# Performance work log

Measured on AMD Instinct MI355X. Metric: run time of the kernel, lower is better.

The kernel has to match this reference:

```python
import jax, jax.numpy as jnp
import numpy as np

LN_EPS = 1e-5
NEG_SLOPE = 0.01  # torch LeakyReLU default
H, D = 16, 64


def _layernorm(x, g, b):
    m = jnp.mean(x, axis=-1, keepdims=True)
    v = jnp.var(x, axis=-1, keepdims=True)
    return (x - m) * jax.lax.rsqrt(v + LN_EPS) * g + b


def _mlp(x, ln_g, ln_b, W1, b1, W2, b2):
    h = _layernorm(x, ln_g, ln_b)
    h = jax.nn.gelu(h @ W1 + b1, approximate=False)
    return h @ W2 + b2


def _gather_nodes(node_msg, edge_index):
    # node_msg: (b,n,c), edge_index: (b,n,k) -> (b,n,k,c)
    return jax.vmap(lambda nm, ei: nm[ei])(node_msg, edge_index)


def setup_inputs() -> dict:
    key = jax.random.key(0)
    ks = jax.random.split(key, 16)
    b, n, k = 2, 1024, 32
    dim, pdim, msg_dim = 512, 256, 256
    s = 0.02
    inp = {
        'node_repr': jax.random.normal(ks[0], (b, n, dim), jnp.float32),
        'edge_repr': jax.random.normal(ks[1], (b, n, k, pdim), jnp.float32),
        'edge_index': jax.random.randint(ks[2], (b, n, k), 0, n, jnp.int32),
        'edge_mask': jax.random.randint(ks[3], (b, n, k), 0, 2, jnp.int32),
        'mask_bw': jnp.ones((b, n, k, 1), jnp.float32),
        'W_edge_msg': s * jax.random.normal(ks[4], (pdim, msg_dim), jnp.float32),
        'W_node_src': s * jax.random.normal(ks[5], (dim, msg_dim), jnp.float32),
        'W_node_tgt': s * jax.random.normal(ks[6], (dim, msg_dim), jnp.float32),
        'msg_ln_g': jnp.ones((msg_dim,), jnp.float32),
        'msg_ln_b': jnp.zeros((msg_dim,), jnp.float32),
        'msg_W1': s * jax.random.normal(ks[7], (msg_dim, 4 * msg_dim), jnp.float32),
        'msg_b1': jnp.zeros((4 * msg_dim,), jnp.float32),
        'msg_W2': s * jax.random.normal(ks[8], (4 * msg_dim, msg_dim), jnp.float32),
        'msg_b2': jnp.zeros((msg_dim,), jnp.float32),
        'W_gate': jnp.zeros((dim, msg_dim), jnp.float32),   # init_weights: zeros
        'b_gate': -jnp.ones((msg_dim,), jnp.float32),       # init_weights: -1
        'W_out': s * jax.random.normal(ks[9], (msg_dim, dim), jnp.float32),
        'W_msg': s * jax.random.normal(ks[10], (msg_dim, msg_dim), jnp.float32),
        'W_attn_bias': s * jax.random.normal(ks[11], (msg_dim, H), jnp.float32),
        'W_gat_value': s * jax.random.normal(ks[12], (msg_dim, H * D), jnp.float32),
        'W_gat_gate': jnp.zeros((dim, H * D), jnp.float32),
        'b_gat_gate': -jnp.ones((H * D,), jnp.float32),
        'W_gat_out': s * jax.random.normal(ks[13], (H * D, dim), jnp.float32),
        'node_ln_g': jnp.ones((dim,), jnp.float32),
        'node_ln_b': jnp.zeros((dim,), jnp.float32),
        'node_W1': s * jax.random.normal(ks[14], (dim, 4 * dim), jnp.float32),
        'node_b1': jnp.zeros((4 * dim,), jnp.float32),
        'node_W2': s * jax.random.normal(ks[15], (4 * dim, dim), jnp.float32),
        'node_b2': jnp.zeros((dim,), jnp.float32),
    }
    return inp


def reference(node_repr, edge_repr, edge_index, edge_mask, mask_bw,
              W_edge_msg, W_node_src, W_node_tgt,
              msg_ln_g, msg_ln_b, msg_W1, msg_b1, msg_W2, msg_b2,
              W_gate, b_gate, W_out,
              W_msg, W_attn_bias, W_gat_value, W_gat_gate, b_gat_gate, W_gat_out,
              node_ln_g, node_ln_b, node_W1, node_b1, node_W2, node_b2):
    b, n, k = edge_index.shape
    em_bool = edge_mask.astype(bool)          # (b,n,k)
    em_f = edge_mask.astype(node_repr.dtype)

    # edge-wise message: edge proj + gathered src node proj + broadcast tgt node proj
    node_msg = node_repr @ W_node_src                      # (b,n,msg)
    msg = edge_repr @ W_edge_msg \
        + _gather_nodes(node_msg, edge_index) * mask_bw \
        + (node_repr @ W_node_tgt)[:, :, None, :]          # (b,n,k,msg)
    msg = _mlp(msg, msg_ln_g, msg_ln_b, msg_W1, msg_b1, msg_W2, msg_b2)
    msg = jnp.where(em_bool[..., None], msg, 0.0)

    # global (mean-pooled, gated) path
    o = (msg * em_f[..., None]).sum(-2) / (em_f.sum(-1, keepdims=True) + 1e-6)
    o = jax.nn.sigmoid(node_repr @ W_gate + b_gate) * o
    dh = o @ W_out                                         # (b,n,dim)

    # GAT path: per-node attention over its k neighbors
    ab = jnp.where(NEG_SLOPE < 1, jax.nn.leaky_relu(msg @ W_msg, NEG_SLOPE), msg) @ W_attn_bias  # (b,n,k,H)
    ab = jnp.where(em_bool[..., None], ab, -jnp.finfo(ab.dtype).max)
    attn = jax.nn.softmax(ab, axis=2)                      # softmax over k
    v = (msg @ W_gat_value).reshape(b, n, k, H, D)
    og = jnp.einsum('bnkh,bnkhd->bnhd', attn, v).reshape(b, n, H * D)
    og = jax.nn.sigmoid(node_repr @ W_gat_gate + b_gat_gate) * og
    dh = dh + og @ W_gat_out

    # residual + node MLP (dropout is identity in eval mode)
    node_repr = node_repr + dh
    node_repr = node_repr + _mlp(node_repr, node_ln_g, node_ln_b, node_W1, node_b1, node_W2, node_b2)
    return node_repr
```

## Files before the change

### kernel.cpp

```cpp
#include <hip/hip_runtime.h>
#include <hip/hip_bf16.h>

typedef unsigned short u16;
typedef short s16x8 __attribute__((ext_vector_type(8)));
typedef float f32x4 __attribute__((ext_vector_type(4)));
typedef float f32x8 __attribute__((ext_vector_type(8)));
typedef u16 u16x8 __attribute__((ext_vector_type(8)));

#define DEV static __device__ __forceinline__

DEV float b2f(u16 u){ unsigned int i=((unsigned int)u)<<16; float f; __builtin_memcpy(&f,&i,4); return f; }
DEV u16 f2b(float x){ __hip_bfloat16 h=__float2bfloat16(x); u16 u; __builtin_memcpy(&u,&h,2); return u; }
DEV f32x4 MFMA(s16x8 a, s16x8 b, f32x4 c){ return __builtin_amdgcn_mfma_f32_16x16x32_bf16(a,b,c,0,0,0); }
DEV s16x8 LD8(const u16* p){ return *(const s16x8*)p; }
DEV float gelu_fast(float x){
  float u = 0.7978845608f*(x + 0.044715f*x*x*x);
  float e = __expf(2.f*u);
  float th = 1.f - 2.f/(e + 1.f);
  return 0.5f*x*(1.f + th);
}
DEV float sigmf(float x){ return 1.0f/(1.0f+__expf(-x)); }

DEV void gload16(const u16* g, u16* l){
  __builtin_amdgcn_global_load_lds((const __attribute__((address_space(1))) void*)g,
                                   (__attribute__((address_space(3))) void*)l, 16, 0, 0);
}

#define WS_WeT   0
#define WS_W1T   65536
#define WS_W2T   327680
#define WS_WmT   589824
#define WS_WvT   655360
#define WS_WoT   917504
#define WS_WgoT  1048576
#define WS_nW1T  1572864
#define WS_nW2T  2621440
#define WS_SrcT  3670016
#define WS_TgtT  3801088
#define WS_GateT 3932160
#define WS_GgT   4063232
#define WS_NM    4587520
#define WS_TGT   5111808
#define WS_GP    5636096
#define WS_GG    6160384
#define WS_MSG   8257536
#define WS_U2    8257536
#define WS_X     10354688
#define WS_Y     12451840
#define WS_WM    25034752
#define WS_U1    33423360
#define WS_YE    33947648
#define WS_H     50724864

struct P13 { const float* p[13]; };
__device__ const int TR_START[14] = {0,16,80,144,160,224,256,384,640,896,928,960,992,1120};
__device__ const int TR_R[13]   = {256,256,1024,256,256,256,1024,512,2048,512,512,512,512};
__device__ const int TR_C[13]   = {256,1024,256,256,1024,512,512,2048,512,256,256,256,1024};
__device__ const int TR_DST[13] = {WS_WeT,WS_W1T,WS_W2T,WS_WmT,WS_WvT,WS_WoT,WS_WgoT,
                                   WS_nW1T,WS_nW2T,WS_SrcT,WS_TgtT,WS_GateT,WS_GgT};

__global__ __launch_bounds__(256) void k_transpose(P13 ps, u16* __restrict__ ws){
  __shared__ alignas(16) u16 Ts[64][72];
  const int t = threadIdx.x;
  int bid = blockIdx.x;
  int mi = 0;
  #pragma unroll 1
  while (bid >= TR_START[mi+1]) ++mi;
  const float* src = ps.p[mi];
  const int R = TR_R[mi], C = TR_C[mi];
  u16* dst = ws + TR_DST[mi];
  const int ti = bid - TR_START[mi];
  const int tcn = C >> 6;
  const int tr = ti / tcn, tc = ti % tcn;
  {
    const int row = t >> 2, cs = (t & 3) * 16;
    const float* sp = src + (tr*64 + row)*C + tc*64 + cs;
    u16x8 a, b;
    #pragma unroll
    for (int i=0;i<8;i++){ a[i]=f2b(sp[i]); b[i]=f2b(sp[8+i]); }
    *(u16x8*)&Ts[row][cs]   = a;
    *(u16x8*)&Ts[row][cs+8] = b;
  }
  __syncthreads();
  {
    const int col = t >> 2, rs = (t & 3) * 16;
    u16x8 a, b;
    #pragma unroll
    for (int i=0;i<8;i++){ a[i]=Ts[rs+i][col]; b[i]=Ts[rs+8+i][col]; }
    u16* dp = dst + (tc*64 + col)*R + tr*64 + rs;
    *(u16x8*)dp = a;
    *(u16x8*)(dp+8) = b;
  }
}

__global__ __launch_bounds__(256) void k_cvtnode(const float* __restrict__ src, u16* __restrict__ dst){
  const int i = (blockIdx.x*256 + threadIdx.x)*8;
  f32x8 v = *(const f32x8*)(src + i);
  u16x8 o;
  #pragma unroll
  for (int j=0;j<8;j++) o[j] = f2b(v[j]);
  *(u16x8*)(dst + i) = o;
}

__global__ __launch_bounds__(256) void k_proj(const float* __restrict__ bgate,
                                              const float* __restrict__ bgg,
                                              u16* __restrict__ ws){
  const int t=threadIdx.x, lid=t&63, w=t>>6, g=lid>>4, q=lid&15;
  const int rb = blockIdx.x, yb = blockIdx.y;
  const u16* nb = ws + WS_H;
  const u16* BT; u16* dst; int Nseg, colbase, act=0; const float* bias=nullptr;
  if (yb < 4){ BT=ws+WS_SrcT;  dst=ws+WS_NM; Nseg=256;  colbase=yb*64; }
  else if (yb < 8){ BT=ws+WS_TgtT;  dst=ws+WS_TGT; Nseg=256; colbase=(yb-4)*64; }
  else if (yb < 12){ BT=ws+WS_GateT; dst=ws+WS_GP; Nseg=256; colbase=(yb-8)*64; act=1; bias=bgate; }
  else { BT=ws+WS_GgT; dst=ws+WS_GG; Nseg=1024; colbase=(yb-12)*64; act=1; bias=bgg; }
  const int wr=(w>>1)*32, wcl=(w&1)*32;
  f32x4 acc[2][2] = {};
  for (int kk=0; kk<512; kk+=32){
    s16x8 af[2], bfr[2];
    #pragma unroll
    for (int i=0;i<2;i++) af[i] = LD8(nb + (rb*64 + wr + i*16 + q)*512 + kk + 8*g);
    #pragma unroll
    for (int j=0;j<2;j++) bfr[j] = LD8(BT + (colbase + wcl + j*16 + q)*512 + kk + 8*g);
    #pragma unroll
    for (int i=0;i<2;i++)
      #pragma unroll
      for (int j=0;j<2;j++) acc[i][j] = MFMA(af[i], bfr[j], acc[i][j]);
  }
  #pragma unroll
  for (int i=0;i<2;i++)
    #pragma unroll
    for (int j=0;j<2;j++)
      #pragma unroll
      for (int r=0;r<4;r++){
        const int row = rb*64 + wr + i*16 + g*4 + r;
        const int col = wcl + j*16 + q;
        float v = acc[i][j][r];
        if (act) v = sigmf(v + bias[colbase+col]);
        dst[row*Nseg + colbase + col] = f2b(v);
      }
}

#define GB_S 528
__global__ __launch_bounds__(256) void k_edgepre(
    const float* __restrict__ edge_repr, const int* __restrict__ edge_index,
    const float* __restrict__ mask_bw,
    const float* __restrict__ ln_g, const float* __restrict__ ln_b,
    u16* __restrict__ ws)
{
  __shared__ alignas(16) char SH[64*GB_S];
  __shared__ float rsS[4][64], rsQ[4][64];
  __shared__ int idxL[64]; __shared__ float mbwL[64];

  const int t=threadIdx.x, lid=t&63, w=t>>6, g=lid>>4, q=lid&15;
  const int R0 = blockIdx.x * 64;
  const int wc = w * 64;
  u16* As = (u16*)SH;
  u16* Bs = (u16*)(SH + 4096);

  if (t < 64){
    idxL[t] = edge_index[R0+t];
    mbwL[t] = mask_bw[R0+t];
  }
  __syncthreads();

  const u16* nm = ws + WS_NM;
  const u16* tg = ws + WS_TGT;
  #pragma unroll
  for (int it=0; it<8; ++it){
    const int v = t + 256*it;
    const int row = v >> 5;
    const int sc  = (v & 31) * 8;
    const int er  = R0 + row;
    const int gnd = er >> 5;
    const int bi  = gnd >> 10;
    const int srow = bi*1024 + idxL[row];
    const float mb = mbwL[row];
    u16x8 nv = *(const u16x8*)(nm + srow*256 + sc);
    u16x8 tv = *(const u16x8*)(tg + gnd*256 + sc);
    u16x8 ov;
    #pragma unroll
    for (int j2=0;j2<8;j2++) ov[j2] = f2b(b2f(nv[j2])*mb + b2f(tv[j2]));
    *(u16x8*)(SH + row*GB_S + 2*sc) = ov;
  }
  __syncthreads();
  f32x4 acc[4][4];
  #pragma unroll
  for (int i=0;i<4;i++)
    #pragma unroll
    for (int r=0;r<4;r++){
      const int row = i*16 + g*4 + r;
      #pragma unroll
      for (int j=0;j<4;j++){
        const int col = wc + j*16 + q;
        acc[i][j][r] = b2f(*(const u16*)(SH + row*GB_S + 2*col));
      }
    }
  for (int kk=0; kk<256; kk+=32){
    __syncthreads();
    {
      const int row = t >> 2, c0 = (t & 3) * 8;
      const float* sp = edge_repr + (R0 + row)*256 + kk + c0;
      f32x8 fv = *(const f32x8*)sp;
      u16x8 av;
      #pragma unroll
      for (int j2=0;j2<8;j2++) av[j2] = f2b(fv[j2]);
      *(u16x8*)(As + row*32 + c0) = av;
    }
    #pragma unroll
    for (int j=0;j<4;j++){
      const int s = t + 256*j;
      const int brow = s >> 2, ko = (s & 3) * 8;
      u16* ldsB = Bs + (w*64 + 256*j)*8;
      gload16(ws + WS_WeT + brow*256 + kk + ko, ldsB);
    }
    __syncthreads();
    s16x8 af[4], bfr[4];
    #pragma unroll
    for (int i=0;i<4;i++) af[i]  = *(const s16x8*)(As + (i*16+q)*32 + g*8);
    #pragma unroll
    for (int j=0;j<4;j++) bfr[j] = *(const s16x8*)(Bs + (wc + j*16 + q)*32 + g*8);
    #pragma unroll
    for (int i=0;i<4;i++)
      #pragma unroll
      for (int j=0;j<4;j++) acc[i][j] = MFMA(af[i], bfr[j], acc[i][j]);
  }
  #pragma unroll
  for (int i=0;i<4;i++)
    #pragma unroll
    for (int r=0;r<4;r++){
      float s=0.f, s2=0.f;
      #pragma unroll
      for (int j=0;j<4;j++){ float v=acc[i][j][r]; s+=v; s2+=v*v; }
      #pragma unroll
      for (int m=1;m<16;m<<=1){ s += __shfl_xor(s,m,64); s2 += __shfl_xor(s2,m,64); }
      if (q==0){ const int row=i*16+g*4+r; rsS[w][row]=s; rsQ[w][row]=s2; }
    }
  __syncthreads();
  u16* Ye = ws + WS_YE;
  #pragma unroll
  for (int i=0;i<4;i++)
    #pragma unroll
    for (int r=0;r<4;r++){
      const int row=i*16+g*4+r;
      const float s  = rsS[0][row]+rsS[1][row]+rsS[2][row]+rsS[3][row];
      const float s2 = rsQ[0][row]+rsQ[1][row]+rsQ[2][row]+rsQ[3][row];
      const float mean = s*(1.f/256.f);
      const float var  = s2*(1.f/256.f) - mean*mean;
      const float rstd = rsqrtf(var + 1e-5f);
      #pragma unroll
      for (int j=0;j<4;j++){
        const int col = wc + j*16 + q;
        Ye[(R0+row)*256 + col] = f2b((acc[i][j][r]-mean)*rstd*ln_g[col] + ln_b[col]);
      }
    }
}

__global__ __launch_bounds__(256) void k_mlp1(const u16* __restrict__ A,
                                              const u16* __restrict__ BT,
                                              const float* __restrict__ b1,
                                              u16* __restrict__ H){
  __shared__ alignas(16) u16 SH2[64*136];
  u16* As = SH2;
  u16* Bs = SH2 + 4096;
  const int t=threadIdx.x, lid=t&63, w=t>>6, g=lid>>4, q=lid&15;
  const int r0 = blockIdx.x*128, n0 = blockIdx.y*128;
  const int wc3 = w*32;
  f32x4 acc[8][2] = {};
  for (int kk=0;kk<256;kk+=32){
    __syncthreads();
    #pragma unroll
    for (int j=0;j<2;j++){
      const int v = t + 256*j;
      const int row = v>>2, sg = (v&3)*8;
      gload16(A  + (r0+row)*256 + kk + sg, As + (w*64 + 256*j)*8);
      gload16(BT + (n0+row)*256 + kk + sg, Bs + (w*64 + 256*j)*8);
    }
    __syncthreads();
    s16x8 bf_[2];
    #pragma unroll
    for (int j=0;j<2;j++) bf_[j] = *(const s16x8*)(Bs + (wc3 + j*16 + q)*32 + g*8);
    #pragma unroll
    for (int i=0;i<8;i++){
      s16x8 af = *(const s16x8*)(As + (i*16+q)*32 + g*8);
      #pragma unroll
      for (int j=0;j<2;j++) acc[i][j] = MFMA(af, bf_[j], acc[i][j]);
    }
  }
  #pragma unroll
  for (int p=0;p<2;p++){
    __syncthreads();
    #pragma unroll
    for (int i2=0;i2<4;i2++)
      #pragma unroll
      for (int j=0;j<2;j++)
        #pragma unroll
        for (int r=0;r<4;r++){
          const int rl = i2*16 + g*4 + r;
          const int cl = wc3 + j*16 + q;
          SH2[rl*136 + cl] = f2b(gelu_fast(acc[p*4+i2][j][r] + b1[n0 + cl]));
        }
    __syncthreads();
    #pragma unroll
    for (int it=0; it<4; ++it){
      const int v = t + 256*it;
      const int rrow = v >> 4, sc = (v & 15)*8;
      *(u16x8*)(H + (r0 + p*64 + rrow)*1024 + n0 + sc) = *(const u16x8*)(SH2 + rrow*136 + sc);
    }
  }
}

__global__ __launch_bounds__(256) void k_mlp2(const u16* __restrict__ A,
                                              const u16* __restrict__ BT,
                                              const float* __restrict__ b2,
                                              const int* __restrict__ em,
                                              u16* __restrict__ msg){
  __shared__ alignas(16) u16 As[128*32];
  __shared__ alignas(16) u16 Bs[128*32];
  __shared__ int emL[128];
  const int t=threadIdx.x, lid=t&63, w=t>>6, g=lid>>4, q=lid&15;
  const int r0 = blockIdx.x*128, n0 = blockIdx.y*128;
  const int wr=(w>>1)*64, wc2=(w&1)*64;
  if (t < 128) emL[t] = em[r0 + t];
  f32x4 acc[4][4] = {};
  for (int kk=0;kk<1024;kk+=32){
    __syncthreads();
    #pragma unroll
    for (int j=0;j<2;j++){
      const int v = t + 256*j;
      const int row = v>>2, sg = (v&3)*8;
      gload16(A  + (r0+row)*1024 + kk + sg, As + (w*64 + 256*j)*8);
      gload16(BT + (n0+row)*1024 + kk + sg, Bs + (w*64 + 256*j)*8);
    }
    __syncthreads();
    s16x8 af[4], bf_[4];
    #pragma unroll
    for (int i=0;i<4;i++) af[i]  = *(const s16x8*)(As + (wr+i*16+q)*32 + g*8);
    #pragma unroll
    for (int j=0;j<4;j++) bf_[j] = *(const s16x8*)(Bs + (wc2+j*16+q)*32 + g*8);
    #pragma unroll
    for (int i=0;i<4;i++)
      #pragma unroll
      for (int j=0;j<4;j++) acc[i][j] = MFMA(af[i], bf_[j], acc[i][j]);
  }
  #pragma unroll
  for (int i=0;i<4;i++)
    #pragma unroll
    for (int j=0;j<4;j++)
      #pragma unroll
      for (int r=0;r<4;r++){
        const int rl  = wr + i*16 + g*4 + r;
        const int col = n0 + wc2 + j*16 + q;
        float v = acc[i][j][r] + b2[col];
        if (!emL[rl]) v = 0.f;
        msg[(r0+rl)*256 + col] = f2b(v);
      }
}

__global__ __launch_bounds__(256) void k_tm(const u16* __restrict__ A,
                                            const u16* __restrict__ BT,
                                            u16* __restrict__ Tm){
  __shared__ alignas(16) u16 SH2[64*136];
  u16* As = SH2;
  u16* Bs = SH2 + 4096;
  const int t=threadIdx.x, lid=t&63, w=t>>6, g=lid>>4, q=lid&15;
  const int r0 = blockIdx.x*128, n0 = blockIdx.y*128;
  const int wc3 = w*32;
  f32x4 acc[8][2] = {};
  for (int kk=0;kk<256;kk+=32){
    __syncthreads();
    #pragma unroll
    for (int j=0;j<2;j++){
      const int v = t + 256*j;
      const int row = v>>2, sg = (v&3)*8;
      gload16(A  + (r0+row)*256 + kk + sg, As + (w*64 + 256*j)*8);
      gload16(BT + (n0+row)*256 + kk + sg, Bs + (w*64 + 256*j)*8);
    }
    __syncthreads();
    s16x8 bf_[2];
    #pragma unroll
    for (int j=0;j<2;j++) bf_[j] = *(const s16x8*)(Bs + (wc3 + j*16 + q)*32 + g*8);
    #pragma unroll
    for (int i=0;i<8;i++){
      s16x8 af = *(const s16x8*)(As + (i*16+q)*32 + g*8);
      #pragma unroll
      for (int j=0;j<2;j++) acc[i][j] = MFMA(af, bf_[j], acc[i][j]);
    }
  }
  #pragma unroll
  for (int p=0;p<2;p++){
    __syncthreads();
    #pragma unroll
    for (int i2=0;i2<4;i2++)
      #pragma unroll
      for (int j=0;j<2;j++)
        #pragma unroll
        for (int r=0;r<4;r++){
          const int rl = i2*16 + g*4 + r;
          const int cl = wc3 + j*16 + q;
          float v = acc[p*4+i2][j][r];
          SH2[rl*136 + cl] = f2b(v > 0.f ? v : 0.01f*v);
        }
    __syncthreads();
    #pragma unroll
    for (int it=0; it<4; ++it){
      const int v = t + 256*it;
      const int rrow = v >> 4, sc = (v & 15)*8;
      *(u16x8*)(Tm + (r0 + p*64 + rrow)*256 + n0 + sc) = *(const u16x8*)(SH2 + rrow*136 + sc);
    }
  }
}

__global__ __launch_bounds__(256) void k_ab(const u16* __restrict__ A,
                                            const float* __restrict__ Wab,
                                            float* __restrict__ AB){
  __shared__ alignas(16) u16 As[128*32];
  __shared__ alignas(16) char WbT[16*528];
  const int t=threadIdx.x, lid=t&63, w=t>>6, g=lid>>4, q=lid&15;
  const int r0 = blockIdx.x*128;
  {
    const float* wr_ = Wab + t*16;
    #pragma unroll
    for (int h=0;h<16;h++) *(u16*)(WbT + h*528 + 2*t) = f2b(wr_[h]);
  }
  f32x4 acc[2] = {};
  for (int kk=0;kk<256;kk+=32){
    __syncthreads();
    #pragma unroll
    for (int j=0;j<2;j++){
      const int s = t + 256*j;
      const int row = s>>2, ko = (s&3)*8;
      gload16(A + (r0+row)*256 + kk + ko, As + (w*64 + 256*j)*8);
    }
    __syncthreads();
    s16x8 bf_ = *(const s16x8*)(WbT + q*528 + 2*(kk + 8*g));
    #pragma unroll
    for (int i=0;i<2;i++){
      s16x8 af = *(const s16x8*)(As + (w*32 + i*16 + q)*32 + g*8);
      acc[i] = MFMA(af, bf_, acc[i]);
    }
  }
  #pragma unroll
  for (int i=0;i<2;i++)
    #pragma unroll
    for (int r=0;r<4;r++){
      const int row = r0 + w*32 + i*16 + g*4 + r;
      AB[row*16 + q] = acc[i][r];
    }
}

#define AM_S 528
#define MT_S 80
__global__ __launch_bounds__(256) void k_attn2(const int* __restrict__ edge_mask,
                                               u16* __restrict__ ws){
  __shared__ alignas(16) char Am[32*AM_S];
  __shared__ alignas(16) char Mt[256*MT_S];
  __shared__ alignas(16) char Pb[16*80];
  __shared__ float Pp[32][16];
  __shared__ int emL[32];
  __shared__ float cntS;

  const int t=threadIdx.x, lid=t&63, w=t>>6, g=lid>>4, q=lid&15;
  const int nd = blockIdx.x;
  const int wc = w*64;
  const u16* msg = ws + WS_MSG + nd*32*256;
  const float* ab = (const float*)(ws + WS_YE) + nd*32*16;

  if (t < 32) emL[t] = edge_mask[nd*32 + t];
  #pragma unroll
  for (int it=0; it<4; ++it){
    const int v = t + 256*it;
    const int row = v >> 5, sc = (v & 31)*8;
    u16x8 val = *(const u16x8*)(msg + row*256 + sc);
    *(u16x8*)(Am + row*AM_S + 2*sc) = val;
  }
  {
    const int k = t >> 4, h = t & 15;
    Pp[k][h]    = ab[k*16 + h];
    Pp[k+16][h] = ab[(k+16)*16 + h];
  }
  __syncthreads();
  if (t == 0){ float c=0.f; for (int k=0;k<32;k++) c += emL[k]?1.f:0.f; cntS=c; }
  {
    const int c = t;
    #pragma unroll 1
    for (int k=0;k<32;k++){
      u16 vv = *(const u16*)(Am + k*AM_S + 2*c);
      *(u16*)(Mt + c*MT_S + 2*k) = vv;
    }
  }
  if (t < 16){
    const int h = t;
    float m = -3.4028235e38f;
    float pv[32];
    for (int k=0;k<32;k++){ pv[k] = emL[k] ? Pp[k][h] : -3.4028235e38f; m = fmaxf(m, pv[k]); }
    float s = 0.f;
    float ev[32];
    for (int k=0;k<32;k++){ ev[k]=__expf(pv[k]-m); s+=ev[k]; }
    const float inv = 1.f/s;
    for (int k=0;k<32;k++) *(u16*)(Pb + h*80 + 2*k) = f2b(ev[k]*inv);
  }
  __syncthreads();
  {
    s16x8 pa = *(const s16x8*)(Pb + q*80 + 2*(8*g));
    f32x4 wmac[4] = {};
    #pragma unroll
    for (int j=0;j<4;j++){
      s16x8 mb = *(const s16x8*)(Mt + (wc + j*16 + q)*MT_S + 2*(8*g));
      wmac[j] = MFMA(pa, mb, wmac[j]);
    }
    u16* wmw = ws + WS_WM;
    #pragma unroll
    for (int j=0;j<4;j++)
      #pragma unroll
      for (int r=0;r<4;r++){
        const int hh = g*4 + r;
        const int col = wc + j*16 + q;
        wmw[hh*(2048*256) + nd*256 + col] = f2b(wmac[j][r]);
      }
  }
  {
    const int c = t;
    float s = 0.f;
    #pragma unroll 1
    for (int k=0;k<32;k++) s += b2f(*(const u16*)(Am + k*AM_S + 2*c));
    const float o = s / (cntS + 1e-6f);
    ws[WS_U1 + nd*256 + c] = f2b(o * b2f(ws[WS_GP + nd*256 + c]));
  }
}

__global__ __launch_bounds__(256) void k_og(u16* __restrict__ ws){
  const int t=threadIdx.x, lid=t&63, w=t>>6, g=lid>>4, q=lid&15;
  const int rb=blockIdx.x, h=blockIdx.y;
  const int wr=(w>>1)*32, wcl=(w&1)*32;
  const u16* A  = ws + WS_WM  + h*(2048*256);
  const u16* BT = ws + WS_WvT;
  f32x4 acc[2][2] = {};
  for (int kk=0;kk<256;kk+=32){
    s16x8 af[2], bfr[2];
    #pragma unroll
    for (int i=0;i<2;i++) af[i] = LD8(A + (rb*64 + wr + i*16 + q)*256 + kk + 8*g);
    #pragma unroll
    for (int j=0;j<2;j++) bfr[j] = LD8(BT + (h*64 + wcl + j*16 + q)*256 + kk + 8*g);
    #pragma unroll
    for (int i=0;i<2;i++)
      #pragma unroll
      for (int j=0;j<2;j++) acc[i][j] = MFMA(af[i], bfr[j], acc[i][j]);
  }
  #pragma unroll
  for (int i=0;i<2;i++)
    #pragma unroll
    for (int j=0;j<2;j++)
      #pragma unroll
      for (int r=0;r<4;r++){
        const int row = rb*64 + wr + i*16 + g*4 + r;
        const int col = h*64 + wcl + j*16 + q;
        const float gv = b2f(ws[WS_GG + row*1024 + col]);
        ws[WS_U2 + row*1024 + col] = f2b(acc[i][j][r] * gv);
      }
}

__global__ __launch_bounds__(256) void k_dh(const float* __restrict__ node_repr, u16* __restrict__ ws){
  const int t=threadIdx.x, lid=t&63, w=t>>6, g=lid>>4, q=lid&15;
  const int rb=blockIdx.x, cb=blockIdx.y*64;
  const int wr=(w>>1)*32, wcl=(w&1)*32;
  float* Xf = (float*)(ws + WS_X);
  f32x4 acc[2][2] = {};
  for (int kk=0;kk<256;kk+=32){
    s16x8 af[2], bfr[2];
    #pragma unroll
    for (int i=0;i<2;i++) af[i] = LD8(ws + WS_U1 + (rb*64 + wr + i*16 + q)*256 + kk + 8*g);
    #pragma unroll
    for (int j=0;j<2;j++) bfr[j] = LD8(ws + WS_WoT + (cb + wcl + j*16 + q)*256 + kk + 8*g);
    #pragma unroll
    for (int i=0;i<2;i++)
      #pragma unroll
      for (int j=0;j<2;j++) acc[i][j] = MFMA(af[i], bfr[j], acc[i][j]);
  }
  for (int kk=0;kk<1024;kk+=32){
    s16x8 af[2], bfr[2];
    #pragma unroll
    for (int i=0;i<2;i++) af[i] = LD8(ws + WS_U2 + (rb*64 + wr + i*16 + q)*1024 + kk + 8*g);
    #pragma unroll
    for (int j=0;j<2;j++) bfr[j] = LD8(ws + WS_WgoT + (cb + wcl + j*16 + q)*1024 + kk + 8*g);
    #pragma unroll
    for (int i=0;i<2;i++)
      #pragma unroll
      for (int j=0;j<2;j++) acc[i][j] = MFMA(af[i], bfr[j], acc[i][j]);
  }
  #pragma unroll
  for (int i=0;i<2;i++)
    #pragma unroll
    for (int j=0;j<2;j++)
      #pragma unroll
      for (int r=0;r<4;r++){
        const int row = rb*64 + wr + i*16 + g*4 + r;
        const int col = cb + wcl + j*16 + q;
        Xf[row*512 + col] = acc[i][j][r] + node_repr[row*512 + col];
      }
}

__global__ __launch_bounds__(256) void k_ln512(const float* __restrict__ g_, const float* __restrict__ b_,
                                               u16* __restrict__ ws){
  const int t=threadIdx.x, wid=t>>6, lane=t&63;
  const int row = blockIdx.x*4 + wid;
  const float* xr = (const float*)(ws + WS_X) + row*512;
  f32x8 xv = *(const f32x8*)(xr + lane*8);
  float s=0.f, s2=0.f;
  #pragma unroll
  for (int i=0;i<8;i++){ s+=xv[i]; s2+=xv[i]*xv[i]; }
  #pragma unroll
  for (int m=1;m<64;m<<=1){ s += __shfl_xor(s,m,64); s2 += __shfl_xor(s2,m,64); }
  const float mean = s*(1.f/512.f);
  const float var  = s2*(1.f/512.f) - mean*mean;
  const float rstd = rsqrtf(var + 1e-5f);
  u16x8 yv;
  #pragma unroll
  for (int i=0;i<8;i++) yv[i] = f2b((xv[i]-mean)*rstd*g_[lane*8+i] + b_[lane*8+i]);
  *(u16x8*)(ws + WS_Y + row*512 + lane*8) = yv;
}

__global__ __launch_bounds__(256) void k_nmlp1(const u16* __restrict__ A,
                                               const u16* __restrict__ BT,
                                               const float* __restrict__ b1,
                                               u16* __restrict__ H){
  __shared__ alignas(16) u16 SH2[64*136];
  u16* As = SH2;
  u16* Bs = SH2 + 4096;
  const int t=threadIdx.x, lid=t&63, w=t>>6, g=lid>>4, q=lid&15;
  const int r0 = blockIdx.x*128, n0 = blockIdx.y*128;
  const int wc3 = w*32;
  f32x4 acc[8][2] = {};
  for (int kk=0;kk<512;kk+=32){
    __syncthreads();
    #pragma unroll
    for (int j=0;j<2;j++){
      const int v = t + 256*j;
      const int row = v>>2, sg = (v&3)*8;
      gload16(A  + (r0+row)*512 + kk + sg, As + (w*64 + 256*j)*8);
      gload16(BT + (n0+row)*512 + kk + sg, Bs + (w*64 + 256*j)*8);
    }
    __syncthreads();
    s16x8 bf_[2];
    #pragma unroll
    for (int j=0;j<2;j++) bf_[j] = *(const s16x8*)(Bs + (wc3 + j*16 + q)*32 + g*8);
    #pragma unroll
    for (int i=0;i<8;i++){
      s16x8 af = *(const s16x8*)(As + (i*16+q)*32 + g*8);
      #pragma unroll
      for (int j=0;j<2;j++) acc[i][j] = MFMA(af, bf_[j], acc[i][j]);
    }
  }
  #pragma unroll
  for (int p=0;p<2;p++){
    __syncthreads();
    #pragma unroll
    for (int i2=0;i2<4;i2++)
      #pragma unroll
      for (int j=0;j<2;j++)
        #pragma unroll
        for (int r=0;r<4;r++){
          const int rl = i2*16 + g*4 + r;
          const int cl = wc3 + j*16 + q;
          SH2[rl*136 + cl] = f2b(gelu_fast(acc[p*4+i2][j][r] + b1[n0 + cl]));
        }
    __syncthreads();
    #pragma unroll
    for (int it=0; it<4; ++it){
      const int v = t + 256*it;
      const int rrow = v >> 4, sc = (v & 15)*8;
      *(u16x8*)(H + (r0 + p*64 + rrow)*2048 + n0 + sc) = *(const u16x8*)(SH2 + rrow*136 + sc);
    }
  }
}

__global__ __launch_bounds__(256) void k_nmlp2(const u16* __restrict__ A,
                                               const u16* __restrict__ BT,
                                               const float* __restrict__ b2,
                                               const float* __restrict__ Xf,
                                               float* __restrict__ out){
  __shared__ alignas(16) u16 As[64*32];
  __shared__ alignas(16) u16 Bs[64*32];
  const int t=threadIdx.x, lid=t&63, w=t>>6, g=lid>>4, q=lid&15;
  const int r0 = blockIdx.x*64, n0 = blockIdx.y*64;
  const int wr=(w>>1)*32, wc2=(w&1)*32;
  f32x4 acc[2][2] = {};
  for (int kk=0;kk<2048;kk+=32){
    __syncthreads();
    {
      const int row = t>>2, sg = (t&3)*8;
      gload16(A  + (r0+row)*2048 + kk + sg, As + (w*64)*8);
      gload16(BT + (n0+row)*2048 + kk + sg, Bs + (w*64)*8);
    }
    __syncthreads();
    s16x8 af[2], bf_[2];
    #pragma unroll
    for (int i=0;i<2;i++) af[i]  = *(const s16x8*)(As + (wr+i*16+q)*32 + g*8);
    #pragma unroll
    for (int j=0;j<2;j++) bf_[j] = *(const s16x8*)(Bs + (wc2+j*16+q)*32 + g*8);
    #pragma unroll
    for (int i=0;i<2;i++)
      #pragma unroll
      for (int j=0;j<2;j++) acc[i][j] = MFMA(af[i], bf_[j], acc[i][j]);
  }
  #pragma unroll
  for (int i=0;i<2;i++)
    #pragma unroll
    for (int j=0;j<2;j++)
      #pragma unroll
      for (int r=0;r<4;r++){
        const int row = r0 + wr + i*16 + g*4 + r;
        const int col = n0 + wc2 + j*16 + q;
        out[row*512 + col] = acc[i][j][r] + b2[col] + Xf[row*512 + col];
      }
}

extern "C" void kernel_launch(void* const* d_in, const int* in_sizes, int n_in,
                              void* d_out, int out_size, void* d_ws, size_t ws_size,
                              hipStream_t stream){
  (void)in_sizes; (void)n_in; (void)out_size; (void)ws_size;
  const float* node_repr = (const float*)d_in[0];
  const float* edge_repr = (const float*)d_in[1];
  const int* edge_index = (const int*)d_in[2];
  const int* edge_mask  = (const int*)d_in[3];
  const float* mask_bw = (const float*)d_in[4];
  u16* ws = (u16*)d_ws;

  P13 ps;
  const int srcIdx[13] = {5,10,12,17,19,16,22,25,27,6,7,14,20};
  for (int i=0;i<13;i++) ps.p[i] = (const float*)d_in[srcIdx[i]];

  hipLaunchKernelGGL(k_transpose, dim3(1120), dim3(256), 0, stream, ps, ws);
  hipLaunchKernelGGL(k_cvtnode, dim3(512), dim3(256), 0, stream, node_repr, ws + WS_H);
  hipLaunchKernelGGL(k_proj, dim3(32,28), dim3(256), 0, stream,
                     (const float*)d_in[15], (const float*)d_in[21], ws);
  hipLaunchKernelGGL(k_edgepre, dim3(1024), dim3(256), 0, stream,
                     edge_repr, edge_index, mask_bw,
                     (const float*)d_in[8], (const float*)d_in[9], ws);
  for (int grp=0; grp<2; ++grp){
    const u16* Ag = ws + WS_YE + grp*32768*256;
    u16* Hg = ws + WS_H;
    u16* msgg = ws + WS_MSG + grp*32768*256;
    const int* emg = edge_mask + grp*32768;
    hipLaunchKernelGGL(k_mlp1, dim3(256,8), dim3(256), 0, stream,
                       Ag, ws + WS_W1T, (const float*)d_in[11], Hg);
    hipLaunchKernelGGL(k_mlp2, dim3(256,2), dim3(256), 0, stream,
                       Hg, ws + WS_W2T, (const float*)d_in[13], emg, msgg);
  }
  hipLaunchKernelGGL(k_tm, dim3(512,2), dim3(256), 0, stream,
                     ws + WS_MSG, ws + WS_WmT, ws + WS_H);
  hipLaunchKernelGGL(k_ab, dim3(512), dim3(256), 0, stream,
                     ws + WS_H, (const float*)d_in[18], (float*)(ws + WS_YE));
  hipLaunchKernelGGL(k_attn2, dim3(2048), dim3(256), 0, stream,
                     edge_mask, ws);
  hipLaunchKernelGGL(k_og, dim3(32,16), dim3(256), 0, stream, ws);
  hipLaunchKernelGGL(k_dh, dim3(32,8), dim3(256), 0, stream, node_repr, ws);
  hipLaunchKernelGGL(k_ln512, dim3(512), dim3(256), 0, stream,
                     (const float*)d_in[23], (const float*)d_in[24], ws);
  hipLaunchKernelGGL(k_nmlp1, dim3(16,16), dim3(256), 0, stream,
                     ws + WS_Y, ws + WS_nW1T, (const float*)d_in[26], ws + WS_H);
  hipLaunchKernelGGL(k_nmlp2, dim3(32,8), dim3(256), 0, stream,
                     ws + WS_H, ws + WS_nW2T, (const float*)d_in[28],
                     (const float*)(ws + WS_X), (float*)d_out);
}
```

Baseline: 351.8 us.

## Double-buffer edge-projection GEMM loads and stage LayerNorm output through LDS

The k_edgepre K-loop now double-buffers its A (edge_repr converted to bf16) and B (W_edge transposed) tiles in shared memory. The next tile's global loads are issued before the current MFMAs, which leaves one barrier per iteration instead of two. The LayerNorm epilogue writes its bf16 results into LDS first and then copies them out with coalesced 16-byte stores, replacing scattered 2-byte global stores. Shared memory per block grows to about 40 KB, which may reduce occupancy.

```diff
diff --git a/kernel.cpp b/kernel.cpp
--- a/kernel.cpp
+++ b/kernel.cpp
@@ -141,21 +141,22 @@
 }
 
 #define GB_S 528
+#define SH_BYTES 40960
 __global__ __launch_bounds__(256) void k_edgepre(
     const float* __restrict__ edge_repr, const int* __restrict__ edge_index,
     const float* __restrict__ mask_bw,
     const float* __restrict__ ln_g, const float* __restrict__ ln_b,
     u16* __restrict__ ws)
 {
-  __shared__ alignas(16) char SH[64*GB_S];
+  __shared__ alignas(16) char SH[SH_BYTES];
   __shared__ float rsS[4][64], rsQ[4][64];
   __shared__ int idxL[64]; __shared__ float mbwL[64];
 
   const int t=threadIdx.x, lid=t&63, w=t>>6, g=lid>>4, q=lid&15;
   const int R0 = blockIdx.x * 64;
   const int wc = w * 64;
-  u16* As = (u16*)SH;
-  u16* Bs = (u16*)(SH + 4096);
+  u16* AsP = (u16*)SH;
+  u16* BsP = (u16*)SH + 4096;
 
   if (t < 64){
     idxL[t] = edge_index[R0+t];
@@ -195,34 +196,55 @@
         acc[i][j][r] = b2f(*(const u16*)(SH + row*GB_S + 2*col));
       }
     }
-  for (int kk=0; kk<256; kk+=32){
-    __syncthreads();
-    {
-      const int row = t >> 2, c0 = (t & 3) * 8;
-      const float* sp = edge_repr + (R0 + row)*256 + kk + c0;
-      f32x8 fv = *(const f32x8*)sp;
-      u16x8 av;
-      #pragma unroll
-      for (int j2=0;j2<8;j2++) av[j2] = f2b(fv[j2]);
-      *(u16x8*)(As + row*32 + c0) = av;
-    }
+  __syncthreads();
+
+  const int arow = t >> 2, ac0 = (t & 3) * 8;
+  {
+    f32x8 fv = *(const f32x8*)(edge_repr + (R0 + arow)*256 + ac0);
+    u16x8 av;
+    #pragma unroll
+    for (int j2=0;j2<8;j2++) av[j2] = f2b(fv[j2]);
+    *(u16x8*)(AsP + arow*32 + ac0) = av;
     #pragma unroll
     for (int j=0;j<4;j++){
       const int s = t + 256*j;
       const int brow = s >> 2, ko = (s & 3) * 8;
-      u16* ldsB = Bs + (w*64 + 256*j)*8;
-      gload16(ws + WS_WeT + brow*256 + kk + ko, ldsB);
-    }
-    __syncthreads();
+      gload16(ws + WS_WeT + brow*256 + ko, BsP + (w*64 + 256*j)*8);
+    }
+  }
+  __syncthreads();
+  int cur = 0;
+  for (int kk=0; kk<256; kk+=32){
+    const int nxt = cur ^ 1;
+    f32x8 fv;
+    if (kk < 224){
+      fv = *(const f32x8*)(edge_repr + (R0 + arow)*256 + kk + 32 + ac0);
+      #pragma unroll
+      for (int j=0;j<4;j++){
+        const int s = t + 256*j;
+        const int brow = s >> 2, ko = (s & 3) * 8;
+        gload16(ws + WS_WeT + brow*256 + kk + 32 + ko, BsP + nxt*8192 + (w*64 + 256*j)*8);
+      }
+    }
+    const u16* AsC = AsP + cur*2048;
+    const u16* BsC = BsP + cur*8192;
     s16x8 af[4], bfr[4];
     #pragma unroll
-    for (int i=0;i<4;i++) af[i]  = *(const s16x8*)(As + (i*16+q)*32 + g*8);
-    #pragma unroll
-    for (int j=0;j<4;j++) bfr[j] = *(const s16x8*)(Bs + (wc + j*16 + q)*32 + g*8);
+    for (int i=0;i<4;i++) af[i]  = *(const s16x8*)(AsC + (i*16+q)*32 + g*8);
+    #pragma unroll
+    for (int j=0;j<4;j++) bfr[j] = *(const s16x8*)(BsC + (wc + j*16 + q)*32 + g*8);
     #pragma unroll
     for (int i=0;i<4;i++)
       #pragma unroll
       for (int j=0;j<4;j++) acc[i][j] = MFMA(af[i], bfr[j], acc[i][j]);
+    if (kk < 224){
+      u16x8 av;
+      #pragma unroll
+      for (int j2=0;j2<8;j2++) av[j2] = f2b(fv[j2]);
+      *(u16x8*)(AsP + nxt*2048 + arow*32 + ac0) = av;
+    }
+    __syncthreads();
+    cur = nxt;
   }
   #pragma unroll
   for (int i=0;i<4;i++)
@@ -236,7 +258,6 @@
       if (q==0){ const int row=i*16+g*4+r; rsS[w][row]=s; rsQ[w][row]=s2; }
     }
   __syncthreads();
-  u16* Ye = ws + WS_YE;
   #pragma unroll
   for (int i=0;i<4;i++)
     #pragma unroll
@@ -250,9 +271,17 @@
       #pragma unroll
       for (int j=0;j<4;j++){
         const int col = wc + j*16 + q;
-        Ye[(R0+row)*256 + col] = f2b((acc[i][j][r]-mean)*rstd*ln_g[col] + ln_b[col]);
-      }
-    }
+        *(u16*)(SH + row*GB_S + 2*col) = f2b((acc[i][j][r]-mean)*rstd*ln_g[col] + ln_b[col]);
+      }
+    }
+  __syncthreads();
+  u16* Ye = ws + WS_YE;
+  #pragma unroll
+  for (int it=0; it<8; ++it){
+    const int v = t + 256*it;
+    const int row = v >> 5, sc = (v & 31)*8;
+    *(u16x8*)(Ye + (R0+row)*256 + sc) = *(const u16x8*)(SH + row*GB_S + 2*sc);
+  }
 }
 
 __global__ __launch_bounds__(256) void k_mlp1(const u16* __restrict__ A,
```

Result: slower. 371.5 us (+5.6%).
